# Optimization experiments

Hardware: AMD Instinct MI355X
Metric: run time of the kernel (lower is better)

## Reference

```python
import jax, jax.numpy as jnp
import numpy as np

D_MODEL = 768
N_HEADS = 12
HEAD_DIM = D_MODEL // N_HEADS


def setup_inputs() -> dict:
    key = jax.random.key(0)
    ks = jax.random.split(key, 9)
    s = 0.02
    B, S = 16, 1024
    return {
        "x": jax.random.normal(ks[0], (B, S, D_MODEL), dtype=jnp.float32),
        "Wq": jax.random.normal(ks[1], (D_MODEL, D_MODEL), dtype=jnp.float32) * s,
        "bq": jnp.zeros((D_MODEL,), dtype=jnp.float32),
        "Wk": jax.random.normal(ks[2], (D_MODEL, D_MODEL), dtype=jnp.float32) * s,
        "bk": jnp.zeros((D_MODEL,), dtype=jnp.float32),
        "Wv": jax.random.normal(ks[3], (D_MODEL, D_MODEL), dtype=jnp.float32) * s,
        "bv": jnp.zeros((D_MODEL,), dtype=jnp.float32),
        "Wc": jax.random.normal(ks[4], (D_MODEL, D_MODEL), dtype=jnp.float32) * s,
        "bc": jnpp if False else jnp.zeros((D_MODEL,), dtype=jnp.float32),
    }


def _split_heads(t):
    # [B, S, D] -> [B, H, S, Dh]
    B, S, _ = t.shape
    return t.reshape(B, S, N_HEADS, HEAD_DIM).transpose(0, 2, 1, 3)


def reference(x, Wq, bq, Wk, bk, Wv, bv, Wc, bc):
    # nn.Linear: y = x @ W.T + b ; here W stored as [out, in]-equivalent square
    q = _split_heads(x @ Wq.T + bq)
    k = _split_heads(x @ Wk.T + bk)
    v = _split_heads(x @ Wv.T + bv)
    scale = jnp.asarray(HEAD_DIM, x.dtype) ** 0.5
    scores = jnp.einsum("bhsd,bhtd->bhst", q, k) / scale  # [B,H,S,S]
    attn = jax.nn.softmax(scores, axis=-1)
    # dropout omitted (deterministic / inference-mode reference)
    ctx = jnp.einsum("bhst,bhtd->bhsd", attn, v)  # [B,H,S,Dh]
    B, H, S, Dh = ctx.shape
    ctx = ctx.transpose(0, 2, 1, 3).reshape(B, S, H * Dh)
    return ctx @ Wc.T + bc
```

## Files before the change

kernel.cpp:

```cpp
#include <hip/hip_runtime.h>
#include <hip/hip_bf16.h>
#include <stdint.h>

#define D_MODEL 768
#define NHEADS 12
#define HDIM 64
#define BATCH 16
#define SEQ 1024
#define MTOK (BATCH*SEQ)
#define LOG2E 1.4426950408889634f

typedef __bf16 bfrag  __attribute__((ext_vector_type(8)));
typedef __bf16 bf16x4 __attribute__((ext_vector_type(4)));
typedef float  f32x4  __attribute__((ext_vector_type(4)));

__device__ __forceinline__ void gload16(const void* g, void* l) {
  __builtin_amdgcn_global_load_lds(
      (const __attribute__((address_space(1))) unsigned int*)g,
      (__attribute__((address_space(3))) unsigned int*)l, 16, 0, 0);
}

__global__ __launch_bounds__(256) void convert_kernel(
    const float* __restrict__ x,
    const float* __restrict__ Wq, const float* __restrict__ Wk,
    const float* __restrict__ Wv, const float* __restrict__ Wc,
    __bf16* __restrict__ xb, __bf16* __restrict__ Wb)
{
  const size_t NX = (size_t)MTOK * D_MODEL;
  const size_t NW = (size_t)D_MODEL * D_MODEL;
  size_t i = ((size_t)blockIdx.x * 256 + threadIdx.x) * 4;
  const float* src; __bf16* dst; size_t off;
  if (i < NX) { src = x; dst = xb; off = i; }
  else {
    size_t wj = i - NX;
    int which = (int)(wj / NW);
    off = wj - (size_t)which * NW;
    src = which == 0 ? Wq : which == 1 ? Wk : which == 2 ? Wv : Wc;
    dst = Wb + (size_t)which * NW;
  }
  f32x4 v = *(const f32x4*)(src + off);
  bf16x4 o;
  o[0] = (__bf16)v[0]; o[1] = (__bf16)v[1]; o[2] = (__bf16)v[2]; o[3] = (__bf16)v[3];
  *(bf16x4*)(dst + off) = o;
}

__global__ __launch_bounds__(256) void qkv_gemm(
    const __bf16* __restrict__ A,
    const __bf16* __restrict__ W,
    const float* __restrict__ bq, const float* __restrict__ bk, const float* __restrict__ bv,
    __bf16* __restrict__ Qb,
    __bf16* __restrict__ Kb,
    __bf16* __restrict__ VTb)
{
  __shared__ __bf16 As[128 * 32];
  __shared__ __bf16 Bs[128 * 32];
  const int tid = threadIdx.x;
  const int lane = tid & 63, w = tid >> 6;
  const int wm = w >> 1, wn = w & 1;
  const int bm = blockIdx.x, bn = blockIdx.y;
  const int r4 = lane >> 2, c8 = (lane & 3) << 3;
  const int l15 = lane & 15, q8 = (lane >> 4) << 3;

  f32x4 acc[4][4];
#pragma unroll
  for (int mt = 0; mt < 4; ++mt)
#pragma unroll
    for (int nt = 0; nt < 4; ++nt) acc[mt][nt] = (f32x4){0.f, 0.f, 0.f, 0.f};

  const size_t am0 = (size_t)bm * 128;
  const size_t bn0 = (size_t)bn * 128;

  for (int kt = 0; kt < 24; ++kt) {
    const int k0 = kt * 32;
#pragma unroll
    for (int i = 0; i < 2; ++i) {
      const int rr = i * 64 + w * 16;
      gload16(A + (am0 + rr + r4) * D_MODEL + k0 + c8, &As[rr * 32]);
      gload16(W + (bn0 + rr + r4) * D_MODEL + k0 + c8, &Bs[rr * 32]);
    }
    __syncthreads();
    bfrag af[4], bf[4];
#pragma unroll
    for (int t = 0; t < 4; ++t) {
      af[t] = *(const bfrag*)&As[(wm * 64 + t * 16 + l15) * 32 + q8];
      bf[t] = *(const bfrag*)&Bs[(wn * 64 + t * 16 + l15) * 32 + q8];
    }
#pragma unroll
    for (int mt = 0; mt < 4; ++mt)
#pragma unroll
      for (int nt = 0; nt < 4; ++nt)
        acc[mt][nt] = __builtin_amdgcn_mfma_f32_16x16x32_bf16(af[mt], bf[nt], acc[mt][nt], 0, 0, 0);
    __syncthreads();
  }

  const int which = bn / 6;
  const int obase = (bn % 6) * 128 + wn * 64;
  const float* bias = which == 0 ? bq : which == 1 ? bk : bv;
  const float qscale = 0.125f * LOG2E;
#pragma unroll
  for (int mt = 0; mt < 4; ++mt) {
    const int row0 = bm * 128 + wm * 64 + mt * 16 + (lane >> 4) * 4;
    const int b = row0 >> 10, s = row0 & 1023;
#pragma unroll
    for (int nt = 0; nt < 4; ++nt) {
      const int o = obase + nt * 16 + l15;
      const float bo = bias[o];
      const int h = o >> 6, d = o & 63;
      const size_t hb = ((size_t)(b * NHEADS + h)) << 16;
      if (which == 2) {
        bf16x4 pv;
#pragma unroll
        for (int r = 0; r < 4; ++r) pv[r] = (__bf16)(acc[mt][nt][r] + bo);
        const int tc = s & 63;
        const size_t addr = hb + (size_t)(s >> 6) * 4096 + (size_t)d * 64
                          + (size_t)((((tc >> 3) ^ (d & 7))) << 3) + (tc & 7);
        *(bf16x4*)&VTb[addr] = pv;
      } else if (which == 0) {
#pragma unroll
        for (int r = 0; r < 4; ++r) {
          const int sr = s + r;
          const size_t addr = hb + (size_t)sr * 64 + (size_t)(((d >> 3) ^ (sr & 7)) << 3) + (d & 7);
          Qb[addr] = (__bf16)((acc[mt][nt][r] + bo) * qscale);
        }
      } else {
#pragma unroll
        for (int r = 0; r < 4; ++r) {
          const int sr = s + r;
          const size_t addr = hb + (size_t)sr * 64 + (size_t)(((d >> 3) ^ (sr & 7)) << 3) + (d & 7);
          Kb[addr] = (__bf16)(acc[mt][nt][r] + bo);
        }
      }
    }
  }
}

__global__ __launch_bounds__(256, 4) void attn_kernel(
    const __bf16* __restrict__ Qb, const __bf16* __restrict__ Kb,
    const __bf16* __restrict__ VTb, __bf16* __restrict__ ctx)
{
  __shared__ __bf16 Ks[2][4096];
  __shared__ __bf16 VTs[2][4096];
  __shared__ __bf16 Ps[4096];
  const int tid = threadIdx.x, lane = tid & 63, w = tid >> 6;
  const int blk = blockIdx.x;
  const int xcd = blk & 7, slot = blk >> 3;
  const int bh = xcd * 24 + (slot >> 4);
  const int qt = slot & 15;
  const int l15 = lane & 15, quad = lane >> 4;
  const int h3 = l15 & 7;
  const size_t base = (size_t)bh << 16;

  const int soff = w * 1024 + lane * 8;

  {
    const __bf16* gq = Qb + base + qt * 4096 + soff;
    const __bf16* gk = Kb + base + soff;
    const __bf16* gv = VTb + base + soff;
    gload16(gq,       &Ps[soff]);
    gload16(gq + 512, &Ps[soff + 512]);
    gload16(gk,       &Ks[0][soff]);
    gload16(gk + 512, &Ks[0][soff + 512]);
    gload16(gv,       &VTs[0][soff]);
    gload16(gv + 512, &VTs[0][soff + 512]);
  }
  __syncthreads();

  const int fq = (w * 16 + l15) * 64 + ((quad ^ h3) << 3);
  bfrag bq0 = *(const bfrag*)&Ps[fq];
  bfrag bq1 = *(const bfrag*)&Ps[fq ^ 32];

  bfrag ones;
#pragma unroll
  for (int i = 0; i < 8; ++i) ones[i] = (__bf16)1.0f;

  f32x4 Oa[4];
  f32x4 lacc = (f32x4){0.f, 0.f, 0.f, 0.f};
#pragma unroll
  for (int nt = 0; nt < 4; ++nt) Oa[nt] = (f32x4){0.f, 0.f, 0.f, 0.f};

  for (int j = 0; j < 16; ++j) {
    const int cb = j & 1, nb = cb ^ 1;
    if (j < 15) {
      const __bf16* gk = Kb + base + (j + 1) * 4096 + soff;
      const __bf16* gv = VTb + base + (j + 1) * 4096 + soff;
      gload16(gk,       &Ks[nb][soff]);
      gload16(gk + 512, &Ks[nb][soff + 512]);
      gload16(gv,       &VTs[nb][soff]);
      gload16(gv + 512, &VTs[nb][soff + 512]);
    }

#pragma unroll
    for (int tt = 0; tt < 4; ++tt) {
      const int fk = (tt * 16 + l15) * 64 + ((quad ^ h3) << 3);
      bfrag ak0 = *(const bfrag*)&Ks[cb][fk];
      bfrag ak1 = *(const bfrag*)&Ks[cb][fk ^ 32];
      f32x4 s4 = (f32x4){0.f, 0.f, 0.f, 0.f};
      s4 = __builtin_amdgcn_mfma_f32_16x16x32_bf16(ak0, bq0, s4, 0, 0, 0);
      s4 = __builtin_amdgcn_mfma_f32_16x16x32_bf16(ak1, bq1, s4, 0, 0, 0);
      bf16x4 p4;
#pragma unroll
      for (int r = 0; r < 4; ++r) p4[r] = (__bf16)exp2f(s4[r]);
      const int u = 2 * tt + (quad >> 1);
      *(bf16x4*)&Ps[(w * 16 + l15) * 64 + ((u ^ h3) << 3) + ((quad & 1) << 2)] = p4;
    }

    const int fp = (w * 16 + l15) * 64 + ((quad ^ h3) << 3);
    bfrag bp0 = *(const bfrag*)&Ps[fp];
    bfrag bp1 = *(const bfrag*)&Ps[fp ^ 32];
    lacc = __builtin_amdgcn_mfma_f32_16x16x32_bf16(ones, bp0, lacc, 0, 0, 0);
    lacc = __builtin_amdgcn_mfma_f32_16x16x32_bf16(ones, bp1, lacc, 0, 0, 0);
#pragma unroll
    for (int nt = 0; nt < 4; ++nt) {
      const int fv = (nt * 16 + l15) * 64 + ((quad ^ h3) << 3);
      bfrag av0 = *(const bfrag*)&VTs[cb][fv];
      bfrag av1 = *(const bfrag*)&VTs[cb][fv ^ 32];
      Oa[nt] = __builtin_amdgcn_mfma_f32_16x16x32_bf16(av0, bp0, Oa[nt], 0, 0, 0);
      Oa[nt] = __builtin_amdgcn_mfma_f32_16x16x32_bf16(av1, bp1, Oa[nt], 0, 0, 0);
    }
    __syncthreads();
  }

  const float inv = 1.0f / lacc[0];

  const int b = bh / NHEADS, h = bh - b * NHEADS;
  const int s = qt * 64 + w * 16 + l15;
  const size_t rowbase = ((size_t)(b * SEQ + s)) * D_MODEL + h * HDIM;
#pragma unroll
  for (int nt = 0; nt < 4; ++nt) {
    bf16x4 o4;
#pragma unroll
    for (int r = 0; r < 4; ++r) o4[r] = (__bf16)(Oa[nt][r] * inv);
    *(bf16x4*)&ctx[rowbase + nt * 16 + quad * 4] = o4;
  }
}

__global__ __launch_bounds__(256) void out_gemm(
    const __bf16* __restrict__ A,
    const __bf16* __restrict__ W,
    const float* __restrict__ bc,
    float* __restrict__ out)
{
  __shared__ __bf16 As[128 * 32];
  __shared__ __bf16 Bs[128 * 32];
  const int tid = threadIdx.x;
  const int lane = tid & 63, w = tid >> 6;
  const int wm = w >> 1, wn = w & 1;
  const int bm = blockIdx.x, bn = blockIdx.y;
  const int r4 = lane >> 2, c8 = (lane & 3) << 3;
  const int l15 = lane & 15, q8 = (lane >> 4) << 3;

  f32x4 acc[4][4];
#pragma unroll
  for (int mt = 0; mt < 4; ++mt)
#pragma unroll
    for (int nt = 0; nt < 4; ++nt) acc[mt][nt] = (f32x4){0.f, 0.f, 0.f, 0.f};

  const size_t am0 = (size_t)bm * 128;
  const size_t bn0 = (size_t)bn * 128;

  for (int kt = 0; kt < 24; ++kt) {
    const int k0 = kt * 32;
#pragma unroll
    for (int i = 0; i < 2; ++i) {
      const int rr = i * 64 + w * 16;
      gload16(A + (am0 + rr + r4) * D_MODEL + k0 + c8, &As[rr * 32]);
      gload16(W + (bn0 + rr + r4) * D_MODEL + k0 + c8, &Bs[rr * 32]);
    }
    __syncthreads();
    bfrag af[4], bf[4];
#pragma unroll
    for (int t = 0; t < 4; ++t) {
      af[t] = *(const bfrag*)&As[(wm * 64 + t * 16 + l15) * 32 + q8];
      bf[t] = *(const bfrag*)&Bs[(wn * 64 + t * 16 + l15) * 32 + q8];
    }
#pragma unroll
    for (int mt = 0; mt < 4; ++mt)
#pragma unroll
      for (int nt = 0; nt < 4; ++nt)
        acc[mt][nt] = __builtin_amdgcn_mfma_f32_16x16x32_bf16(af[mt], bf[nt], acc[mt][nt], 0, 0, 0);
    __syncthreads();
  }

#pragma unroll
  for (int mt = 0; mt < 4; ++mt) {
    const int row0 = bm * 128 + wm * 64 + mt * 16 + (lane >> 4) * 4;
#pragma unroll
    for (int nt = 0; nt < 4; ++nt) {
      const int o = bn * 128 + wn * 64 + nt * 16 + l15;
      const float bo = bc[o];
#pragma unroll
      for (int r = 0; r < 4; ++r)
        out[(size_t)(row0 + r) * D_MODEL + o] = acc[mt][nt][r] + bo;
    }
  }
}

extern "C" void kernel_launch(void* const* d_in, const int* in_sizes, int n_in,
                              void* d_out, int out_size, void* d_ws, size_t ws_size,
                              hipStream_t stream)
{
  const float* x  = (const float*)d_in[0];
  const float* Wq = (const float*)d_in[1];
  const float* bq = (const float*)d_in[2];
  const float* Wk = (const float*)d_in[3];
  const float* bk = (const float*)d_in[4];
  const float* Wv = (const float*)d_in[5];
  const float* bv = (const float*)d_in[6];
  const float* Wc = (const float*)d_in[7];
  const float* bc = (const float*)d_in[8];
  float* out = (float*)d_out;

  char* ws = (char*)d_ws;
  __bf16* xb  = (__bf16*)(ws);
  __bf16* Wb  = (__bf16*)(ws + 25165824);
  __bf16* Qb  = (__bf16*)(ws + 29884416);
  __bf16* Kb  = (__bf16*)(ws + 55050240);
  __bf16* VTb = (__bf16*)(ws + 80216064);
  __bf16* ctx = xb;

  convert_kernel<<<14592, 256, 0, stream>>>(x, Wq, Wk, Wv, Wc, xb, Wb);
  qkv_gemm<<<dim3(128, 18), 256, 0, stream>>>(xb, Wb, bq, bk, bv, Qb, Kb, VTb);
  attn_kernel<<<3072, 256, 0, stream>>>(Qb, Kb, VTb, ctx);
  out_gemm<<<dim3(128, 6), 256, 0, stream>>>(ctx, Wb + 3 * 589824, bc, out);
}
```

Before: 294.6 us.

## Split attention KV tile across warps, keep P in registers, reduce partial outputs

The attention kernel now gives each warp 16 keys of the 64-key tile for all 64 queries, rather than 16 queries over all keys. Each warp computes scores with the 32-wide MFMA and feeds the exp'd probabilities straight from registers into 16x16x16 MFMAs against V, removing the P round trip through shared memory and the ones-vector MFMA used for row sums. Row sums are accumulated in scalar registers, and the four per-warp partial outputs are reduced through shared memory at the end. This raises register use (16 accumulator tiles), so occupancy is lowered to 3 blocks, and it adds an extra reduction phase with several barriers.

```diff
diff --git a/kernel.cpp b/kernel.cpp
--- a/kernel.cpp
+++ b/kernel.cpp
@@ -13,11 +13,30 @@
 typedef __bf16 bfrag  __attribute__((ext_vector_type(8)));
 typedef __bf16 bf16x4 __attribute__((ext_vector_type(4)));
 typedef float  f32x4  __attribute__((ext_vector_type(4)));
+typedef short  s16x4  __attribute__((ext_vector_type(4)));
 
 __device__ __forceinline__ void gload16(const void* g, void* l) {
   __builtin_amdgcn_global_load_lds(
       (const __attribute__((address_space(1))) unsigned int*)g,
       (__attribute__((address_space(3))) unsigned int*)l, 16, 0, 0);
+}
+
+__device__ __forceinline__ float fexp2(float x) {
+#if __has_builtin(__builtin_amdgcn_exp2f)
+  return __builtin_amdgcn_exp2f(x);
+#else
+  return exp2f(x);
+#endif
+}
+
+__device__ __forceinline__ void mfma16(bf16x4 a, bf16x4 b, f32x4& c) {
+#if __has_builtin(__builtin_amdgcn_mfma_f32_16x16x16bf16_1k)
+  c = __builtin_amdgcn_mfma_f32_16x16x16bf16_1k(
+        __builtin_bit_cast(s16x4, a), __builtin_bit_cast(s16x4, b), c, 0, 0, 0);
+#else
+  asm volatile("s_nop 1\n\tv_mfma_f32_16x16x16_bf16 %0, %1, %2, %0\n\ts_nop 7\n\ts_nop 7"
+               : "+v"(c) : "v"(a), "v"(b));
+#endif
 }
 
 __global__ __launch_bounds__(256) void convert_kernel(
@@ -134,13 +153,13 @@
   }
 }
 
-__global__ __launch_bounds__(256, 4) void attn_kernel(
+__global__ __launch_bounds__(256, 3) void attn_kernel(
     const __bf16* __restrict__ Qb, const __bf16* __restrict__ Kb,
     const __bf16* __restrict__ VTb, __bf16* __restrict__ ctx)
 {
-  __shared__ __bf16 Ks[2][4096];
-  __shared__ __bf16 VTs[2][4096];
-  __shared__ __bf16 Ps[4096];
+  __shared__ __align__(16) char smem_raw[32768];
+  __shared__ float rs[256];
+  __bf16* S = (__bf16*)smem_raw;
   const int tid = threadIdx.x, lane = tid & 63, w = tid >> 6;
   const int blk = blockIdx.x;
   const int xcd = blk & 7, slot = blk >> 3;
@@ -156,81 +175,125 @@
     const __bf16* gq = Qb + base + qt * 4096 + soff;
     const __bf16* gk = Kb + base + soff;
     const __bf16* gv = VTb + base + soff;
-    gload16(gq,       &Ps[soff]);
-    gload16(gq + 512, &Ps[soff + 512]);
-    gload16(gk,       &Ks[0][soff]);
-    gload16(gk + 512, &Ks[0][soff + 512]);
-    gload16(gv,       &VTs[0][soff]);
-    gload16(gv + 512, &VTs[0][soff + 512]);
+    gload16(gq,       S + 12288 + soff);
+    gload16(gq + 512, S + 12288 + soff + 512);
+    gload16(gk,       S + soff);
+    gload16(gk + 512, S + soff + 512);
+    gload16(gv,       S + 8192 + soff);
+    gload16(gv + 512, S + 8192 + soff + 512);
   }
   __syncthreads();
 
-  const int fq = (w * 16 + l15) * 64 + ((quad ^ h3) << 3);
-  bfrag bq0 = *(const bfrag*)&Ps[fq];
-  bfrag bq1 = *(const bfrag*)&Ps[fq ^ 32];
-
-  bfrag ones;
-#pragma unroll
-  for (int i = 0; i < 8; ++i) ones[i] = (__bf16)1.0f;
-
-  f32x4 Oa[4];
-  f32x4 lacc = (f32x4){0.f, 0.f, 0.f, 0.f};
-#pragma unroll
-  for (int nt = 0; nt < 4; ++nt) Oa[nt] = (f32x4){0.f, 0.f, 0.f, 0.f};
+  bfrag bq[4][2];
+#pragma unroll
+  for (int q2 = 0; q2 < 4; ++q2) {
+    const int fq = 12288 + (q2 * 16 + l15) * 64 + ((quad ^ h3) << 3);
+    bq[q2][0] = *(const bfrag*)&S[fq];
+    bq[q2][1] = *(const bfrag*)&S[fq ^ 32];
+  }
+  __syncthreads();
+
+  f32x4 Oa[4][4];
+#pragma unroll
+  for (int dt = 0; dt < 4; ++dt)
+#pragma unroll
+    for (int q2 = 0; q2 < 4; ++q2) Oa[dt][q2] = (f32x4){0.f, 0.f, 0.f, 0.f};
+  float sacc[4] = {0.f, 0.f, 0.f, 0.f};
+
+  const int fk  = (w * 16 + l15) * 64 + ((quad ^ h3) << 3);
+  const int fvb = l15 * 64 + (((w * 2 + (quad >> 1)) ^ h3) << 3) + ((quad & 1) << 2);
 
   for (int j = 0; j < 16; ++j) {
     const int cb = j & 1, nb = cb ^ 1;
     if (j < 15) {
       const __bf16* gk = Kb + base + (j + 1) * 4096 + soff;
       const __bf16* gv = VTb + base + (j + 1) * 4096 + soff;
-      gload16(gk,       &Ks[nb][soff]);
-      gload16(gk + 512, &Ks[nb][soff + 512]);
-      gload16(gv,       &VTs[nb][soff]);
-      gload16(gv + 512, &VTs[nb][soff + 512]);
-    }
-
-#pragma unroll
-    for (int tt = 0; tt < 4; ++tt) {
-      const int fk = (tt * 16 + l15) * 64 + ((quad ^ h3) << 3);
-      bfrag ak0 = *(const bfrag*)&Ks[cb][fk];
-      bfrag ak1 = *(const bfrag*)&Ks[cb][fk ^ 32];
+      gload16(gk,       S + nb * 4096 + soff);
+      gload16(gk + 512, S + nb * 4096 + soff + 512);
+      gload16(gv,       S + 8192 + nb * 4096 + soff);
+      gload16(gv + 512, S + 8192 + nb * 4096 + soff + 512);
+    }
+    const __bf16* Kc = S + cb * 4096;
+    const __bf16* Vc = S + 8192 + cb * 4096;
+
+    bfrag ak0 = *(const bfrag*)&Kc[fk];
+    bfrag ak1 = *(const bfrag*)&Kc[fk ^ 32];
+    bf16x4 av[4];
+#pragma unroll
+    for (int dt = 0; dt < 4; ++dt) av[dt] = *(const bf16x4*)&Vc[dt * 1024 + fvb];
+
+    bf16x4 pb[4];
+#pragma unroll
+    for (int q2 = 0; q2 < 4; ++q2) {
       f32x4 s4 = (f32x4){0.f, 0.f, 0.f, 0.f};
-      s4 = __builtin_amdgcn_mfma_f32_16x16x32_bf16(ak0, bq0, s4, 0, 0, 0);
-      s4 = __builtin_amdgcn_mfma_f32_16x16x32_bf16(ak1, bq1, s4, 0, 0, 0);
-      bf16x4 p4;
-#pragma unroll
-      for (int r = 0; r < 4; ++r) p4[r] = (__bf16)exp2f(s4[r]);
-      const int u = 2 * tt + (quad >> 1);
-      *(bf16x4*)&Ps[(w * 16 + l15) * 64 + ((u ^ h3) << 3) + ((quad & 1) << 2)] = p4;
-    }
-
-    const int fp = (w * 16 + l15) * 64 + ((quad ^ h3) << 3);
-    bfrag bp0 = *(const bfrag*)&Ps[fp];
-    bfrag bp1 = *(const bfrag*)&Ps[fp ^ 32];
-    lacc = __builtin_amdgcn_mfma_f32_16x16x32_bf16(ones, bp0, lacc, 0, 0, 0);
-    lacc = __builtin_amdgcn_mfma_f32_16x16x32_bf16(ones, bp1, lacc, 0, 0, 0);
-#pragma unroll
-    for (int nt = 0; nt < 4; ++nt) {
-      const int fv = (nt * 16 + l15) * 64 + ((quad ^ h3) << 3);
-      bfrag av0 = *(const bfrag*)&VTs[cb][fv];
-      bfrag av1 = *(const bfrag*)&VTs[cb][fv ^ 32];
-      Oa[nt] = __builtin_amdgcn_mfma_f32_16x16x32_bf16(av0, bp0, Oa[nt], 0, 0, 0);
-      Oa[nt] = __builtin_amdgcn_mfma_f32_16x16x32_bf16(av1, bp1, Oa[nt], 0, 0, 0);
-    }
-    __syncthreads();
-  }
-
-  const float inv = 1.0f / lacc[0];
-
+      s4 = __builtin_amdgcn_mfma_f32_16x16x32_bf16(ak0, bq[q2][0], s4, 0, 0, 0);
+      s4 = __builtin_amdgcn_mfma_f32_16x16x32_bf16(ak1, bq[q2][1], s4, 0, 0, 0);
+      const float p0 = fexp2(s4[0]), p1 = fexp2(s4[1]);
+      const float p2 = fexp2(s4[2]), p3 = fexp2(s4[3]);
+      sacc[q2] += (p0 + p1) + (p2 + p3);
+      bf16x4 pv;
+      pv[0] = (__bf16)p0; pv[1] = (__bf16)p1; pv[2] = (__bf16)p2; pv[3] = (__bf16)p3;
+      pb[q2] = pv;
+    }
+
+#pragma unroll
+    for (int dt = 0; dt < 4; ++dt)
+#pragma unroll
+      for (int q2 = 0; q2 < 4; ++q2)
+        mfma16(av[dt], pb[q2], Oa[dt][q2]);
+
+    __syncthreads();
+  }
+
+  float vsum[4];
+#pragma unroll
+  for (int q2 = 0; q2 < 4; ++q2) {
+    float v = sacc[q2];
+    v += __shfl_xor(v, 16);
+    v += __shfl_xor(v, 32);
+    vsum[q2] = v;
+  }
+  if (quad == 0) {
+#pragma unroll
+    for (int q2 = 0; q2 < 4; ++q2) rs[w * 64 + q2 * 16 + l15] = vsum[q2];
+  }
+  __syncthreads();
+  if (w == 0) {
+    const float tot = rs[lane] + rs[64 + lane] + rs[128 + lane] + rs[192 + lane];
+    rs[lane] = 1.0f / tot;
+  }
+  __syncthreads();
+
+  float* fs = (float*)smem_raw;
   const int b = bh / NHEADS, h = bh - b * NHEADS;
-  const int s = qt * 64 + w * 16 + l15;
-  const size_t rowbase = ((size_t)(b * SEQ + s)) * D_MODEL + h * HDIM;
-#pragma unroll
-  for (int nt = 0; nt < 4; ++nt) {
-    bf16x4 o4;
-#pragma unroll
-    for (int r = 0; r < 4; ++r) o4[r] = (__bf16)(Oa[nt][r] * inv);
-    *(bf16x4*)&ctx[rowbase + nt * 16 + quad * 4] = o4;
+  const int off = l15 * 16 + quad * 4;
+#pragma unroll
+  for (int rd = 0; rd < 2; ++rd) {
+#pragma unroll
+    for (int dl = 0; dl < 2; ++dl)
+#pragma unroll
+      for (int q2 = 0; q2 < 4; ++q2)
+        *(f32x4*)&fs[w * 2048 + dl * 1024 + q2 * 256 + off] = Oa[rd * 2 + dl][q2];
+    __syncthreads();
+#pragma unroll
+    for (int e = 0; e < 2; ++e) {
+      const int idx = w * 2 + e;
+      const int dl = idx >> 2, q2 = idx & 3;
+      const int tb = dl * 1024 + q2 * 256 + off;
+      f32x4 s0 = *(const f32x4*)&fs[tb];
+      f32x4 s1 = *(const f32x4*)&fs[2048 + tb];
+      f32x4 s2 = *(const f32x4*)&fs[4096 + tb];
+      f32x4 s3 = *(const f32x4*)&fs[6144 + tb];
+      f32x4 sum = (s0 + s1) + (s2 + s3);
+      const float li = rs[q2 * 16 + l15];
+      const int dt = rd * 2 + dl;
+      const int s = qt * 64 + q2 * 16 + l15;
+      bf16x4 o4;
+#pragma unroll
+      for (int r = 0; r < 4; ++r) o4[r] = (__bf16)(sum[r] * li);
+      *(bf16x4*)&ctx[((size_t)(b * SEQ + s)) * D_MODEL + h * HDIM + dt * 16 + quad * 4] = o4;
+    }
+    __syncthreads();
   }
 }
 
```

After: 290.0 us. No clear change (-1.6%).
